# Kernel tuning notes

Hardware: AMD Instinct MI355X
Metric: run time of the kernel (lower is better)

## Reference

```python
import jax, jax.numpy as jnp
import numpy as np

K = 3        # kernel_size
STRIDE = 1
PAD = 1
DIL = 1


def setup_inputs() -> dict:
    key = jax.random.key(0)
    ks = jax.random.split(key, 5)
    B, C, H, W, O = 4, 64, 128, 128, 64
    x = jax.random.normal(ks[0], (B, C, H, W), jnp.float32)
    # small offset-conv weights -> offsets of a few pixels (realistic trained regime)
    offset_w = jax.random.normal(ks[1], (2 * K * K, C, K, K), jnp.float32) * 0.01
    offset_b = jax.random.normal(ks[2], (2 * K * K,), jnp.float32) * 0.01
    weight = jax.random.normal(ks[3], (O, C, K, K), jnp.float32)
    bias = jax.random.normal(ks[4], (O,), jnp.float32)
    return {"x": x, "offset_w": offset_w, "offset_b": offset_b,
            "weight": weight, "bias": bias}


def _conv2d(x, w, b):
    y = jax.lax.conv_general_dilated(
        x, w, window_strides=(STRIDE, STRIDE),
        padding=[(PAD, PAD), (PAD, PAD)],
        dimension_numbers=("NCHW", "OIHW", "NCHW"))
    return y + b[None, :, None, None]


def _deform_conv2d(x, offset, weight, bias):
    B, C, H, W = x.shape
    O = weight.shape[0]
    KK = K * K
    Ho, Wo = offset.shape[2], offset.shape[3]
    # offset channels ordered (y, x) per kernel tap: [B, KK, 2, Ho, Wo]
    off = offset.reshape(B, KK, 2, Ho, Wo)
    kyy, kxx = jnp.meshgrid(jnp.arange(K) * DIL, jnp.arange(K) * DIL, indexing="ij")
    kyy = kyy.reshape(KK).astype(x.dtype)
    kxx = kxx.reshape(KK).astype(x.dtype)
    base_y = (jnp.arange(Ho) * STRIDE - PAD).astype(x.dtype)
    base_x = (jnp.arange(Wo) * STRIDE - PAD).astype(x.dtype)
    # sampling positions [B, KK, Ho, Wo]
    py = base_y[None, None, :, None] + kyy[None, :, None, None] + off[:, :, 0]
    px = base_x[None, None, None, :] + kxx[None, :, None, None] + off[:, :, 1]

    y0 = jnp.floor(py); x0 = jnp.floor(px)
    y1 = y0 + 1.0;      x1 = x0 + 1.0
    wy1 = py - y0; wy0 = 1.0 - wy1
    wx1 = px - x0; wx0 = 1.0 - wx1

    xf = x.reshape(B, C, H * W)

    def corner(yc, xc):
        valid = (yc >= 0) & (yc < H) & (xc >= 0) & (xc < W)  # zero padding outside
        idx = (jnp.clip(yc, 0, H - 1) * W + jnp.clip(xc, 0, W - 1)).astype(jnp.int32)
        g = jax.vmap(lambda xb, ib: xb[:, ib.reshape(-1)])(xf, idx)  # [B, C, KK*Ho*Wo]
        g = g.reshape(B, C, KK, Ho, Wo)
        return g * valid[:, None].astype(x.dtype)

    val = (corner(y0, x0) * (wy0 * wx0)[:, None]
         + corner(y0, x1) * (wy0 * wx1)[:, None]
         + corner(y1, x0) * (wy1 * wx0)[:, None]
         + corner(y1, x1) * (wy1 * wx1)[:, None])  # [B, C, KK, Ho, Wo]

    out = jnp.einsum("bckhw,ock->bohw", val, weight.reshape(O, C, KK))
    return out + bias[None, :, None, None]


def reference(x, offset_w, offset_b, weight, bias):
    offset = _conv2d(x, offset_w, offset_b)
    return _deform_conv2d(x, offset, weight, bias)
```

## Files before the change

### kernel.cpp

```cpp
#include <hip/hip_runtime.h>

#define B_   4
#define C_   64
#define O_   64
#define H_   128
#define W_   128
#define HW_  (H_ * W_)
#define KK_  9
#define M_   18

typedef short  short8  __attribute__((ext_vector_type(8)));
typedef float  floatx4 __attribute__((ext_vector_type(4)));
typedef unsigned short ushort4v __attribute__((ext_vector_type(4)));
typedef unsigned short ushort8v __attribute__((ext_vector_type(8)));

static __device__ __forceinline__ unsigned short f2bf(float f) {
    unsigned int u = __float_as_uint(f);
    u += 0x7FFFu + ((u >> 16) & 1u);
    return (unsigned short)(u >> 16);
}
static __device__ __forceinline__ float bf2f(unsigned short s) {
    return __uint_as_float((unsigned int)s << 16);
}

__global__ void repack(const float* __restrict__ w, const float* __restrict__ ow,
                       unsigned short* __restrict__ wtb,
                       unsigned short* __restrict__ owtb) {
    int i = blockIdx.x * blockDim.x + threadIdx.x;
    if (i < 576 * O_) {
        int o = i / 576, r = i % 576;
        int tap = r >> 6, c = r & 63;
        wtb[i] = f2bf(w[o * 576 + c * 9 + tap]);
    }
    if (i < 9 * 32 * 64) {
        int tap = i >> 11, m = (i >> 6) & 31, c = i & 63;
        owtb[i] = (m < M_) ? f2bf(ow[m * 576 + c * 9 + tap]) : (unsigned short)0;
    }
}

__global__ __launch_bounds__(256) void xpose(const float* __restrict__ x,
                                             unsigned short* __restrict__ xT) {
    __shared__ unsigned short T[128][72];
    const int tid = threadIdx.x;
    const int y = blockIdx.x & (H_ - 1);
    const int b = blockIdx.x >> 7;
    const float* xby = x + (size_t)b * C_ * HW_ + y * W_;
    for (int i = tid; i < C_ * W_; i += 256) {
        const int c = i >> 7, xc = i & 127;
        T[xc][c] = f2bf(xby[(size_t)c * HW_ + xc]);
    }
    __syncthreads();
    unsigned short* dst = xT + (size_t)b * (4 * HW_ * 16) + y * (W_ * 16);
    for (int j = tid; j < 2048; j += 256) {
        const int g  = j >> 9;
        const int x8 = (j >> 2) & 127;
        const int c0 = (j & 3) * 4;
        const ushort4v pk = *(const ushort4v*)&T[x8][g * 16 + c0];
        *(ushort4v*)&dst[(size_t)g * (HW_ * 16) + x8 * 16 + c0] = pk;
    }
}

__global__ __launch_bounds__(256, 4) void dcn_fused(
        const unsigned short* __restrict__ xT,
        const unsigned short* __restrict__ owtb, const float* __restrict__ ob,
        const unsigned short* __restrict__ wtb, const float* __restrict__ bias,
        float* __restrict__ out) {
    __shared__ union {
        unsigned short P[3][66][72];
        unsigned short vals[64][192];
        float ep[4][16][65];
    } u;
    __shared__ float offs[M_ * 64];

    const int tid    = threadIdx.x;
    const int lane   = tid & 63;
    const int wslot  = __builtin_amdgcn_readfirstlane(tid >> 6);
    const int lane15 = lane & 15;
    const int quad   = lane >> 4;

    const int g    = blockIdx.x;
    const int xcd  = g & 7;
    const int slot = g >> 3;
    const int ho   = xcd * 16 + (slot >> 3);
    const int b    = (slot >> 1) & 3;
    const int wo_base = (slot & 1) << 6;

    const unsigned short* xTb = xT + (size_t)b * (4 * HW_ * 16);

    #pragma unroll
    for (int it = 0; it < 3; ++it) {
        const int t  = it * 4 + wslot;
        const int ky = t >> 2, cgp = t & 3;
        const int y  = ho - 1 + ky;
        const bool yv = (unsigned)y < (unsigned)H_;
        const unsigned short* src = xTb + (size_t)cgp * (HW_ * 16) + y * (W_ * 16);
        #pragma unroll
        for (int pass = 0; pass < 2; ++pass) {
            const int r = pass * 64 + lane;
            if (r < 66) {
                const int cx = wo_base + r - 1;
                ushort8v p0 = {0, 0, 0, 0, 0, 0, 0, 0};
                ushort8v p1 = {0, 0, 0, 0, 0, 0, 0, 0};
                if (yv && (unsigned)cx < (unsigned)W_) {
                    p0 = *(const ushort8v*)&src[cx * 16];
                    p1 = *(const ushort8v*)&src[cx * 16 + 8];
                }
                *(ushort8v*)&u.P[ky][r][cgp * 16]     = p0;
                *(ushort8v*)&u.P[ky][r][cgp * 16 + 8] = p1;
            }
        }
    }
    __syncthreads();

    {
        floatx4 oa0 = (floatx4){0.f, 0.f, 0.f, 0.f};
        floatx4 oa1 = (floatx4){0.f, 0.f, 0.f, 0.f};
        const int pxt = wslot;
        #pragma unroll
        for (int ky = 0; ky < 3; ++ky) {
            #pragma unroll
            for (int kx = 0; kx < 3; ++kx) {
                const int tap = ky * 3 + kx;
                #pragma unroll
                for (int ks = 0; ks < 2; ++ks) {
                    const int kk = ks * 32 + quad * 8;
                    const short8 af =
                        *(const short8*)&u.P[ky][pxt * 16 + lane15 + kx][kk];
                    const short8 bf0 =
                        *(const short8*)&owtb[(size_t)(tap * 32 + lane15) * 64 + kk];
                    const short8 bf1 =
                        *(const short8*)&owtb[(size_t)(tap * 32 + 16 + lane15) * 64 + kk];
                    oa0 = __builtin_amdgcn_mfma_f32_16x16x32_bf16(af, bf0, oa0, 0, 0, 0);
                    oa1 = __builtin_amdgcn_mfma_f32_16x16x32_bf16(af, bf1, oa1, 0, 0, 0);
                }
            }
        }
        *(floatx4*)&offs[lane15 * 64 + pxt * 16 + quad * 4] = oa0;
        if (lane15 < 2)
            *(floatx4*)&offs[(16 + lane15) * 64 + pxt * 16 + quad * 4] = oa1;
    }
    __syncthreads();

    const int obase = wslot * 16;
    const int cg    = lane & 3;
    const int px16  = lane >> 2;
    floatx4 acc[4];
    #pragma unroll
    for (int t = 0; t < 4; ++t) acc[t] = (floatx4){0.f, 0.f, 0.f, 0.f};
    const unsigned short* xTw = xTb + (size_t)wslot * (HW_ * 16);

    for (int chunk = 0; chunk < 3; ++chunk) {
        #pragma unroll
        for (int tl = 0; tl < 3; ++tl) {
            const int k  = chunk * 3 + tl;
            const int ky = k / 3, kx = k % 3;
            const float oby = ob[2 * k], obx = ob[2 * k + 1];
            #pragma unroll
            for (int pxt = 0; pxt < 4; ++pxt) {
                const int px = pxt * 16 + px16;
                const float offy = offs[(2 * k)     * 64 + px] + oby;
                const float offx = offs[(2 * k + 1) * 64 + px] + obx;
                const float py  = (float)(ho - 1 + ky) + offy;
                const float pxx = (float)(wo_base - 1 + kx + px) + offx;
                const float fy = floorf(py), fx = floorf(pxx);
                const int y0 = (int)fy, x0 = (int)fx;
                const int y1 = y0 + 1,  x1 = x0 + 1;
                const float wy1 = py - fy,  wy0 = 1.f - wy1;
                const float wx1 = pxx - fx, wx0 = 1.f - wx1;
                const bool y0v = (unsigned)y0 < (unsigned)H_;
                const bool y1v = (unsigned)y1 < (unsigned)H_;
                const bool x0v = (unsigned)x0 < (unsigned)W_;
                const bool x1v = (unsigned)x1 < (unsigned)W_;
                const float w00 = (y0v && x0v) ? wy0 * wx0 : 0.f;
                const float w01 = (y0v && x1v) ? wy0 * wx1 : 0.f;
                const float w10 = (y1v && x0v) ? wy1 * wx0 : 0.f;
                const float w11 = (y1v && x1v) ? wy1 * wx1 : 0.f;
                const int ry0 = min(max(y0, 0), H_ - 1);
                const int ry1 = min(max(y1, 0), H_ - 1);
                const int cx0 = min(max(x0, 0), W_ - 1);
                const int cx1 = min(max(x1, 0), W_ - 1);
                const int a00 = (ry0 * W_ + cx0) * 16 + cg * 4;
                const int a01 = (ry0 * W_ + cx1) * 16 + cg * 4;
                const int a10 = (ry1 * W_ + cx0) * 16 + cg * 4;
                const int a11 = (ry1 * W_ + cx1) * 16 + cg * 4;
                const ushort4v q00 = *(const ushort4v*)&xTw[a00];
                const ushort4v q01 = *(const ushort4v*)&xTw[a01];
                const ushort4v q10 = *(const ushort4v*)&xTw[a10];
                const ushort4v q11 = *(const ushort4v*)&xTw[a11];
                ushort4v pk;
                #pragma unroll
                for (int q = 0; q < 4; ++q) {
                    const float val = bf2f(q00[q]) * w00 + bf2f(q01[q]) * w01
                                    + bf2f(q10[q]) * w10 + bf2f(q11[q]) * w11;
                    pk[q] = f2bf(val);
                }
                const int cidx =
                    tl * 8 + (((wslot << 1) + (cg >> 1)) ^ (px & 7));
                *(ushort4v*)&u.vals[px][cidx * 8 + (cg & 1) * 4] = pk;
            }
        }
        __syncthreads();

        const unsigned short* wrow =
            wtb + (size_t)(obase + lane15) * 576 + chunk * 192;
        #pragma unroll
        for (int ks = 0; ks < 6; ++ks) {
            const int kk = ks * 32 + quad * 8;
            const short8 bfrag = *(const short8*)(wrow + kk);
            const int ca  = (ks * 4 + quad) >> 3;
            const int cbr = ((ks * 4 + quad) & 7) ^ (lane15 & 7);
            #pragma unroll
            for (int t = 0; t < 4; ++t) {
                const int row = t * 16 + lane15;
                const short8 afrag =
                    *(const short8*)&u.vals[row][(ca * 8 + cbr) * 8];
                acc[t] = __builtin_amdgcn_mfma_f32_16x16x32_bf16(
                             afrag, bfrag, acc[t], 0, 0, 0);
            }
        }
        __syncthreads();
    }

    #pragma unroll
    for (int t = 0; t < 4; ++t)
        #pragma unroll
        for (int r = 0; r < 4; ++r)
            u.ep[wslot][lane15][t * 16 + quad * 4 + r] = acc[t][r];
    __syncthreads();
    #pragma unroll
    for (int oi = 0; oi < 16; ++oi) {
        const int o = obase + oi;
        out[(size_t)(b * O_ + o) * HW_ + ho * W_ + wo_base + lane] =
            u.ep[wslot][oi][lane] + bias[o];
    }
}

extern "C" void kernel_launch(void* const* d_in, const int* in_sizes, int n_in,
                              void* d_out, int out_size, void* d_ws, size_t ws_size,
                              hipStream_t stream) {
    const float* x    = (const float*)d_in[0];
    const float* ow   = (const float*)d_in[1];
    const float* ob   = (const float*)d_in[2];
    const float* w    = (const float*)d_in[3];
    const float* bias = (const float*)d_in[4];
    float* out = (float*)d_out;

    unsigned short* wtb  = (unsigned short*)d_ws;
    unsigned short* owtb = wtb + 576 * O_;
    unsigned short* xT   = owtb + 9 * 32 * 64;

    repack<<<(576 * O_ + 255) / 256, 256, 0, stream>>>(w, ow, wtb, owtb);
    xpose<<<B_ * H_, 256, 0, stream>>>(x, xT);
    dcn_fused<<<B_ * H_ * (W_ / 64), 256, 0, stream>>>(xT, owtb, ob, wtb, bias, out);
}
```

Before: 129.8 us.

## Regroup bf16 input into 4-channel planes, merge prep kernels, load corner pairs

Changes the transposed bf16 input layout from 16-channel groups to 4-channel groups, so that each gather lane reads two adjacent x-pixels with one 16-byte load per row instead of four separate 8-byte corner loads. Border columns are handled by clamping the base x to W-2 and remapping the bilinear weights. The repack and transpose kernels are merged into a single launch. The offsets buffer is moved into the shared-memory union, which needs an extra barrier, and the occupancy hint in launch bounds is removed. The tile prologue now issues more, smaller loads.

```diff
diff --git a/kernel.cpp b/kernel.cpp
--- a/kernel.cpp
+++ b/kernel.cpp
@@ -8,6 +8,7 @@
 #define HW_  (H_ * W_)
 #define KK_  9
 #define M_   18
+#define GHW  (HW_ * 4)
 
 typedef short  short8  __attribute__((ext_vector_type(8)));
 typedef float  floatx4 __attribute__((ext_vector_type(4)));
@@ -23,54 +24,57 @@
     return __uint_as_float((unsigned int)s << 16);
 }
 
-__global__ void repack(const float* __restrict__ w, const float* __restrict__ ow,
-                       unsigned short* __restrict__ wtb,
-                       unsigned short* __restrict__ owtb) {
-    int i = blockIdx.x * blockDim.x + threadIdx.x;
-    if (i < 576 * O_) {
-        int o = i / 576, r = i % 576;
-        int tap = r >> 6, c = r & 63;
-        wtb[i] = f2bf(w[o * 576 + c * 9 + tap]);
-    }
-    if (i < 9 * 32 * 64) {
-        int tap = i >> 11, m = (i >> 6) & 31, c = i & 63;
-        owtb[i] = (m < M_) ? f2bf(ow[m * 576 + c * 9 + tap]) : (unsigned short)0;
-    }
-}
-
-__global__ __launch_bounds__(256) void xpose(const float* __restrict__ x,
-                                             unsigned short* __restrict__ xT) {
-    __shared__ unsigned short T[128][72];
-    const int tid = threadIdx.x;
-    const int y = blockIdx.x & (H_ - 1);
-    const int b = blockIdx.x >> 7;
-    const float* xby = x + (size_t)b * C_ * HW_ + y * W_;
-    for (int i = tid; i < C_ * W_; i += 256) {
-        const int c = i >> 7, xc = i & 127;
-        T[xc][c] = f2bf(xby[(size_t)c * HW_ + xc]);
-    }
-    __syncthreads();
-    unsigned short* dst = xT + (size_t)b * (4 * HW_ * 16) + y * (W_ * 16);
-    for (int j = tid; j < 2048; j += 256) {
-        const int g  = j >> 9;
-        const int x8 = (j >> 2) & 127;
-        const int c0 = (j & 3) * 4;
-        const ushort4v pk = *(const ushort4v*)&T[x8][g * 16 + c0];
-        *(ushort4v*)&dst[(size_t)g * (HW_ * 16) + x8 * 16 + c0] = pk;
-    }
-}
-
-__global__ __launch_bounds__(256, 4) void dcn_fused(
+__global__ __launch_bounds__(256) void prep(
+        const float* __restrict__ x, const float* __restrict__ w,
+        const float* __restrict__ ow, unsigned short* __restrict__ xT,
+        unsigned short* __restrict__ wtb, unsigned short* __restrict__ owtb) {
+    const int blk = blockIdx.x;
+    if (blk < 512) {
+        __shared__ unsigned short T[128][72];
+        const int tid = threadIdx.x;
+        const int y = blk & (H_ - 1);
+        const int b = blk >> 7;
+        const float* xby = x + (size_t)b * C_ * HW_ + y * W_;
+        for (int i = tid; i < C_ * W_; i += 256) {
+            const int c = i >> 7, xc = i & 127;
+            T[xc][c] = f2bf(xby[(size_t)c * HW_ + xc]);
+        }
+        __syncthreads();
+        unsigned short* dst = xT + (size_t)b * 16 * GHW + y * (W_ * 4);
+        for (int j = tid; j < 2048; j += 256) {
+            const int G  = j >> 7;
+            const int x8 = j & 127;
+            const ushort4v pk = *(const ushort4v*)&T[x8][G * 4];
+            *(ushort4v*)&dst[(size_t)G * GHW + x8 * 4] = pk;
+        }
+    } else {
+        const int i = (blk - 512) * 256 + threadIdx.x;
+        if (i < 576 * O_) {
+            int o = i / 576, r = i % 576;
+            int tap = r >> 6, c = r & 63;
+            wtb[i] = f2bf(w[o * 576 + c * 9 + tap]);
+        }
+        if (i < 9 * 32 * 64) {
+            int tap = i >> 11, m = (i >> 6) & 31, c = i & 63;
+            owtb[i] = (m < M_) ? f2bf(ow[m * 576 + c * 9 + tap])
+                               : (unsigned short)0;
+        }
+    }
+}
+
+__global__ __launch_bounds__(256) void dcn_fused(
         const unsigned short* __restrict__ xT,
         const unsigned short* __restrict__ owtb, const float* __restrict__ ob,
         const unsigned short* __restrict__ wtb, const float* __restrict__ bias,
         float* __restrict__ out) {
     __shared__ union {
         unsigned short P[3][66][72];
-        unsigned short vals[64][192];
+        struct {
+            unsigned short vals[64][192];
+            float offs[M_ * 64];
+        } bv;
         float ep[4][16][65];
     } u;
-    __shared__ float offs[M_ * 64];
 
     const int tid    = threadIdx.x;
     const int lane   = tid & 63;
@@ -85,29 +89,31 @@
     const int b    = (slot >> 1) & 3;
     const int wo_base = (slot & 1) << 6;
 
-    const unsigned short* xTb = xT + (size_t)b * (4 * HW_ * 16);
-
-    #pragma unroll
-    for (int it = 0; it < 3; ++it) {
+    const unsigned short* xT4b = xT + (size_t)b * 16 * GHW;
+
+    #pragma unroll
+    for (int it = 0; it < 12; ++it) {
         const int t  = it * 4 + wslot;
-        const int ky = t >> 2, cgp = t & 3;
+        const int ky = t >> 4, G = t & 15;
         const int y  = ho - 1 + ky;
         const bool yv = (unsigned)y < (unsigned)H_;
-        const unsigned short* src = xTb + (size_t)cgp * (HW_ * 16) + y * (W_ * 16);
-        #pragma unroll
-        for (int pass = 0; pass < 2; ++pass) {
-            const int r = pass * 64 + lane;
-            if (r < 66) {
-                const int cx = wo_base + r - 1;
-                ushort8v p0 = {0, 0, 0, 0, 0, 0, 0, 0};
-                ushort8v p1 = {0, 0, 0, 0, 0, 0, 0, 0};
-                if (yv && (unsigned)cx < (unsigned)W_) {
-                    p0 = *(const ushort8v*)&src[cx * 16];
-                    p1 = *(const ushort8v*)&src[cx * 16 + 8];
-                }
-                *(ushort8v*)&u.P[ky][r][cgp * 16]     = p0;
-                *(ushort8v*)&u.P[ky][r][cgp * 16 + 8] = p1;
-            }
+        const int yc = min(max(y, 0), H_ - 1);
+        const unsigned short* src = xT4b + ((size_t)G * HW_ + yc * W_) * 4;
+        {
+            const int r  = lane;
+            const int cx = wo_base + r - 1;
+            ushort4v p = {0, 0, 0, 0};
+            if (yv && (unsigned)cx < (unsigned)W_)
+                p = *(const ushort4v*)&src[cx * 4];
+            *(ushort4v*)&u.P[ky][r][G * 4] = p;
+        }
+        if (lane < 2) {
+            const int r  = 64 + lane;
+            const int cx = wo_base + r - 1;
+            ushort4v p = {0, 0, 0, 0};
+            if (yv && (unsigned)cx < (unsigned)W_)
+                p = *(const ushort4v*)&src[cx * 4];
+            *(ushort4v*)&u.P[ky][r][G * 4] = p;
         }
     }
     __syncthreads();
@@ -135,9 +141,10 @@
                 }
             }
         }
-        *(floatx4*)&offs[lane15 * 64 + pxt * 16 + quad * 4] = oa0;
+        __syncthreads();
+        *(floatx4*)&u.bv.offs[lane15 * 64 + pxt * 16 + quad * 4] = oa0;
         if (lane15 < 2)
-            *(floatx4*)&offs[(16 + lane15) * 64 + pxt * 16 + quad * 4] = oa1;
+            *(floatx4*)&u.bv.offs[(16 + lane15) * 64 + pxt * 16 + quad * 4] = oa1;
     }
     __syncthreads();
 
@@ -147,7 +154,7 @@
     floatx4 acc[4];
     #pragma unroll
     for (int t = 0; t < 4; ++t) acc[t] = (floatx4){0.f, 0.f, 0.f, 0.f};
-    const unsigned short* xTw = xTb + (size_t)wslot * (HW_ * 16);
+    const unsigned short* xTw = xT4b + (size_t)(wslot * 4 + cg) * GHW;
 
     for (int chunk = 0; chunk < 3; ++chunk) {
         #pragma unroll
@@ -158,8 +165,8 @@
             #pragma unroll
             for (int pxt = 0; pxt < 4; ++pxt) {
                 const int px = pxt * 16 + px16;
-                const float offy = offs[(2 * k)     * 64 + px] + oby;
-                const float offx = offs[(2 * k + 1) * 64 + px] + obx;
+                const float offy = u.bv.offs[(2 * k)     * 64 + px] + oby;
+                const float offx = u.bv.offs[(2 * k + 1) * 64 + px] + obx;
                 const float py  = (float)(ho - 1 + ky) + offy;
                 const float pxx = (float)(wo_base - 1 + kx + px) + offx;
                 const float fy = floorf(py), fx = floorf(pxx);
@@ -175,28 +182,25 @@
                 const float w01 = (y0v && x1v) ? wy0 * wx1 : 0.f;
                 const float w10 = (y1v && x0v) ? wy1 * wx0 : 0.f;
                 const float w11 = (y1v && x1v) ? wy1 * wx1 : 0.f;
+                const int bx  = min(max(x0, 0), W_ - 2);
                 const int ry0 = min(max(y0, 0), H_ - 1);
                 const int ry1 = min(max(y1, 0), H_ - 1);
-                const int cx0 = min(max(x0, 0), W_ - 1);
-                const int cx1 = min(max(x1, 0), W_ - 1);
-                const int a00 = (ry0 * W_ + cx0) * 16 + cg * 4;
-                const int a01 = (ry0 * W_ + cx1) * 16 + cg * 4;
-                const int a10 = (ry1 * W_ + cx0) * 16 + cg * 4;
-                const int a11 = (ry1 * W_ + cx1) * 16 + cg * 4;
-                const ushort4v q00 = *(const ushort4v*)&xTw[a00];
-                const ushort4v q01 = *(const ushort4v*)&xTw[a01];
-                const ushort4v q10 = *(const ushort4v*)&xTw[a10];
-                const ushort4v q11 = *(const ushort4v*)&xTw[a11];
+                const float cA0 = (x0 == bx) ? w00 : ((x1 == bx) ? w01 : 0.f);
+                const float cB0 = (x1 == bx + 1) ? w01 : ((x0 == bx + 1) ? w00 : 0.f);
+                const float cA1 = (x0 == bx) ? w10 : ((x1 == bx) ? w11 : 0.f);
+                const float cB1 = (x1 == bx + 1) ? w11 : ((x0 == bx + 1) ? w10 : 0.f);
+                const ushort8v p0 = *(const ushort8v*)&xTw[(ry0 * W_ + bx) * 4];
+                const ushort8v p1 = *(const ushort8v*)&xTw[(ry1 * W_ + bx) * 4];
                 ushort4v pk;
                 #pragma unroll
                 for (int q = 0; q < 4; ++q) {
-                    const float val = bf2f(q00[q]) * w00 + bf2f(q01[q]) * w01
-                                    + bf2f(q10[q]) * w10 + bf2f(q11[q]) * w11;
+                    const float val = bf2f(p0[q])     * cA0 + bf2f(p0[4 + q]) * cB0
+                                    + bf2f(p1[q])     * cA1 + bf2f(p1[4 + q]) * cB1;
                     pk[q] = f2bf(val);
                 }
                 const int cidx =
                     tl * 8 + (((wslot << 1) + (cg >> 1)) ^ (px & 7));
-                *(ushort4v*)&u.vals[px][cidx * 8 + (cg & 1) * 4] = pk;
+                *(ushort4v*)&u.bv.vals[px][cidx * 8 + (cg & 1) * 4] = pk;
             }
         }
         __syncthreads();
@@ -213,7 +217,7 @@
             for (int t = 0; t < 4; ++t) {
                 const int row = t * 16 + lane15;
                 const short8 afrag =
-                    *(const short8*)&u.vals[row][(ca * 8 + cbr) * 8];
+                    *(const short8*)&u.bv.vals[row][(ca * 8 + cbr) * 8];
                 acc[t] = __builtin_amdgcn_mfma_f32_16x16x32_bf16(
                              afrag, bfrag, acc[t], 0, 0, 0);
             }
@@ -249,7 +253,6 @@
     unsigned short* owtb = wtb + 576 * O_;
     unsigned short* xT   = owtb + 9 * 32 * 64;
 
-    repack<<<(576 * O_ + 255) / 256, 256, 0, stream>>>(w, ow, wtb, owtb);
-    xpose<<<B_ * H_, 256, 0, stream>>>(x, xT);
+    prep<<<512 + 144, 256, 0, stream>>>(x, w, ow, xT, wtb, owtb);
     dcn_fused<<<B_ * H_ * (W_ / 64), 256, 0, stream>>>(xT, owtb, ob, wtb, bias, out);
 }
```

Result: slower. 142.8 us (+10.0%).

## Merge prep kernels, pre-swizzle weights into MFMA fragment order, share LDS for offsets

Applied to the files above, without the earlier changes.

Folds the weight repack and the x transpose into one prep launch, which drops a kernel launch. Both weight tensors are now stored in MFMA fragment order, so each lane reads one contiguous 16-byte vector. The offsets buffer moves into the shared-memory union next to vals, which cuts LDS per block, and launch bounds rise to 5 blocks per CU to raise occupancy. This costs an extra barrier before the offsets are written, needed because offs now aliases the P staging area.

```diff
diff --git a/kernel.cpp b/kernel.cpp
--- a/kernel.cpp
+++ b/kernel.cpp
@@ -23,54 +23,73 @@
     return __uint_as_float((unsigned int)s << 16);
 }
 
-__global__ void repack(const float* __restrict__ w, const float* __restrict__ ow,
-                       unsigned short* __restrict__ wtb,
-                       unsigned short* __restrict__ owtb) {
-    int i = blockIdx.x * blockDim.x + threadIdx.x;
-    if (i < 576 * O_) {
-        int o = i / 576, r = i % 576;
-        int tap = r >> 6, c = r & 63;
-        wtb[i] = f2bf(w[o * 576 + c * 9 + tap]);
-    }
-    if (i < 9 * 32 * 64) {
-        int tap = i >> 11, m = (i >> 6) & 31, c = i & 63;
-        owtb[i] = (m < M_) ? f2bf(ow[m * 576 + c * 9 + tap]) : (unsigned short)0;
-    }
-}
-
-__global__ __launch_bounds__(256) void xpose(const float* __restrict__ x,
-                                             unsigned short* __restrict__ xT) {
-    __shared__ unsigned short T[128][72];
-    const int tid = threadIdx.x;
-    const int y = blockIdx.x & (H_ - 1);
-    const int b = blockIdx.x >> 7;
-    const float* xby = x + (size_t)b * C_ * HW_ + y * W_;
-    for (int i = tid; i < C_ * W_; i += 256) {
-        const int c = i >> 7, xc = i & 127;
-        T[xc][c] = f2bf(xby[(size_t)c * HW_ + xc]);
-    }
-    __syncthreads();
-    unsigned short* dst = xT + (size_t)b * (4 * HW_ * 16) + y * (W_ * 16);
-    for (int j = tid; j < 2048; j += 256) {
-        const int g  = j >> 9;
-        const int x8 = (j >> 2) & 127;
-        const int c0 = (j & 3) * 4;
-        const ushort4v pk = *(const ushort4v*)&T[x8][g * 16 + c0];
-        *(ushort4v*)&dst[(size_t)g * (HW_ * 16) + x8 * 16 + c0] = pk;
-    }
-}
-
-__global__ __launch_bounds__(256, 4) void dcn_fused(
+__global__ __launch_bounds__(256) void prep(
+        const float* __restrict__ x, const float* __restrict__ w,
+        const float* __restrict__ ow, unsigned short* __restrict__ xT,
+        unsigned short* __restrict__ wtbf, unsigned short* __restrict__ owtbf) {
+    const int blk = blockIdx.x;
+    if (blk < 512) {
+        __shared__ unsigned short T[128][72];
+        const int tid = threadIdx.x;
+        const int y = blk & (H_ - 1);
+        const int b = blk >> 7;
+        const float* xby = x + (size_t)b * C_ * HW_ + y * W_;
+        for (int i = tid; i < C_ * W_; i += 256) {
+            const int c = i >> 7, xc = i & 127;
+            T[xc][c] = f2bf(xby[(size_t)c * HW_ + xc]);
+        }
+        __syncthreads();
+        unsigned short* dst = xT + (size_t)b * (4 * HW_ * 16) + y * (W_ * 16);
+        for (int j = tid; j < 2048; j += 256) {
+            const int g  = j >> 9;
+            const int x8 = (j >> 2) & 127;
+            const int c0 = (j & 3) * 4;
+            const ushort4v pk = *(const ushort4v*)&T[x8][g * 16 + c0];
+            *(ushort4v*)&dst[(size_t)g * (HW_ * 16) + x8 * 16 + c0] = pk;
+        }
+    } else if (blk < 530) {
+        const int i = (blk - 512) * 256 + threadIdx.x;
+        const int lane = i & 63, rest = i >> 6;
+        const int ot = rest & 3, cks = rest >> 2;
+        const int chunk = cks / 6, ks = cks % 6;
+        const int o = ot * 16 + (lane & 15);
+        const int kbase = chunk * 192 + ks * 32 + (lane >> 4) * 8;
+        ushort8v pk;
+        #pragma unroll
+        for (int j = 0; j < 8; ++j) {
+            const int k = kbase + j;
+            pk[j] = f2bf(w[o * 576 + (k & 63) * 9 + (k >> 6)]);
+        }
+        *(ushort8v*)&wtbf[(size_t)i * 8] = pk;
+    } else {
+        const int i = (blk - 530) * 256 + threadIdx.x;
+        const int lane = i & 63, rest = i >> 6;
+        const int tile = rest & 1, tks = rest >> 1;
+        const int tap = tks >> 1, ks = tks & 1;
+        const int m = tile * 16 + (lane & 15);
+        const int cb = ks * 32 + (lane >> 4) * 8;
+        ushort8v pk;
+        #pragma unroll
+        for (int j = 0; j < 8; ++j)
+            pk[j] = (m < M_) ? f2bf(ow[m * 576 + (cb + j) * 9 + tap])
+                             : (unsigned short)0;
+        *(ushort8v*)&owtbf[(size_t)i * 8] = pk;
+    }
+}
+
+__global__ __launch_bounds__(256, 5) void dcn_fused(
         const unsigned short* __restrict__ xT,
-        const unsigned short* __restrict__ owtb, const float* __restrict__ ob,
-        const unsigned short* __restrict__ wtb, const float* __restrict__ bias,
+        const unsigned short* __restrict__ owtbf, const float* __restrict__ ob,
+        const unsigned short* __restrict__ wtbf, const float* __restrict__ bias,
         float* __restrict__ out) {
     __shared__ union {
         unsigned short P[3][66][72];
-        unsigned short vals[64][192];
+        struct {
+            unsigned short vals[64][192];
+            float offs[M_ * 64];
+        } bv;
         float ep[4][16][65];
     } u;
-    __shared__ float offs[M_ * 64];
 
     const int tid    = threadIdx.x;
     const int lane   = tid & 63;
@@ -126,18 +145,19 @@
                     const int kk = ks * 32 + quad * 8;
                     const short8 af =
                         *(const short8*)&u.P[ky][pxt * 16 + lane15 + kx][kk];
-                    const short8 bf0 =
-                        *(const short8*)&owtb[(size_t)(tap * 32 + lane15) * 64 + kk];
+                    const int fb = ((tap * 2 + ks) * 2) * 64 + lane;
+                    const short8 bf0 = *(const short8*)&owtbf[(size_t)fb * 8];
                     const short8 bf1 =
-                        *(const short8*)&owtb[(size_t)(tap * 32 + 16 + lane15) * 64 + kk];
+                        *(const short8*)&owtbf[(size_t)(fb + 64) * 8];
                     oa0 = __builtin_amdgcn_mfma_f32_16x16x32_bf16(af, bf0, oa0, 0, 0, 0);
                     oa1 = __builtin_amdgcn_mfma_f32_16x16x32_bf16(af, bf1, oa1, 0, 0, 0);
                 }
             }
         }
-        *(floatx4*)&offs[lane15 * 64 + pxt * 16 + quad * 4] = oa0;
+        __syncthreads();
+        *(floatx4*)&u.bv.offs[lane15 * 64 + pxt * 16 + quad * 4] = oa0;
         if (lane15 < 2)
-            *(floatx4*)&offs[(16 + lane15) * 64 + pxt * 16 + quad * 4] = oa1;
+            *(floatx4*)&u.bv.offs[(16 + lane15) * 64 + pxt * 16 + quad * 4] = oa1;
     }
     __syncthreads();
 
@@ -158,8 +178,8 @@
             #pragma unroll
             for (int pxt = 0; pxt < 4; ++pxt) {
                 const int px = pxt * 16 + px16;
-                const float offy = offs[(2 * k)     * 64 + px] + oby;
-                const float offx = offs[(2 * k + 1) * 64 + px] + obx;
+                const float offy = u.bv.offs[(2 * k)     * 64 + px] + oby;
+                const float offx = u.bv.offs[(2 * k + 1) * 64 + px] + obx;
                 const float py  = (float)(ho - 1 + ky) + offy;
                 const float pxx = (float)(wo_base - 1 + kx + px) + offx;
                 const float fy = floorf(py), fx = floorf(pxx);
@@ -196,24 +216,22 @@
                 }
                 const int cidx =
                     tl * 8 + (((wslot << 1) + (cg >> 1)) ^ (px & 7));
-                *(ushort4v*)&u.vals[px][cidx * 8 + (cg & 1) * 4] = pk;
-            }
-        }
-        __syncthreads();
-
-        const unsigned short* wrow =
-            wtb + (size_t)(obase + lane15) * 576 + chunk * 192;
+                *(ushort4v*)&u.bv.vals[px][cidx * 8 + (cg & 1) * 4] = pk;
+            }
+        }
+        __syncthreads();
+
         #pragma unroll
         for (int ks = 0; ks < 6; ++ks) {
-            const int kk = ks * 32 + quad * 8;
-            const short8 bfrag = *(const short8*)(wrow + kk);
+            const short8 bfrag = *(const short8*)
+                &wtbf[(size_t)(((chunk * 6 + ks) * 4 + wslot) * 64 + lane) * 8];
             const int ca  = (ks * 4 + quad) >> 3;
             const int cbr = ((ks * 4 + quad) & 7) ^ (lane15 & 7);
             #pragma unroll
             for (int t = 0; t < 4; ++t) {
                 const int row = t * 16 + lane15;
                 const short8 afrag =
-                    *(const short8*)&u.vals[row][(ca * 8 + cbr) * 8];
+                    *(const short8*)&u.bv.vals[row][(ca * 8 + cbr) * 8];
                 acc[t] = __builtin_amdgcn_mfma_f32_16x16x32_bf16(
                              afrag, bfrag, acc[t], 0, 0, 0);
             }
@@ -245,11 +263,10 @@
     const float* bias = (const float*)d_in[4];
     float* out = (float*)d_out;
 
-    unsigned short* wtb  = (unsigned short*)d_ws;
-    unsigned short* owtb = wtb + 576 * O_;
-    unsigned short* xT   = owtb + 9 * 32 * 64;
-
-    repack<<<(576 * O_ + 255) / 256, 256, 0, stream>>>(w, ow, wtb, owtb);
-    xpose<<<B_ * H_, 256, 0, stream>>>(x, xT);
-    dcn_fused<<<B_ * H_ * (W_ / 64), 256, 0, stream>>>(xT, owtb, ob, wtb, bias, out);
-}
+    unsigned short* wtbf  = (unsigned short*)d_ws;
+    unsigned short* owtbf = wtbf + 4608 * 8;
+    unsigned short* xT    = owtbf + 2304 * 8;
+
+    prep<<<539, 256, 0, stream>>>(x, w, ow, xT, wtbf, owtbf);
+    dcn_fused<<<B_ * H_ * (W_ / 64), 256, 0, stream>>>(xT, owtbf, ob, wtbf, bias, out);
+}
```

After: 117.9 us. 9.2% less time.
